# Kernel tuning notes

Hardware: AMD Instinct MI355X
Metric: run time of the kernel (lower is better)

The kernel has to match this reference:

```python
import jax, jax.numpy as jnp
import numpy as np

T = 32          # chain length (init arg)
K = 2048        # particles per timestep (Ks)
RES = 0.5       # observed scalar (init buffer)
LIKE_STD = 1.0  # likelihood std (init arg)
LOG2PI = float(np.log(2.0 * np.pi))


def _logpdf(x, mu, std):
    # Normal(mu, std).log_prob(x)
    z = (x - mu) / std
    return -0.5 * z * z - jnp.log(std) - 0.5 * LOG2PI


def logmmmeanexp(X, Y):
    # log( exp(X) @ exp(Y) / X.shape[1] ), numerically stabilized exactly as the torch code
    x = jnp.max(X, axis=1, keepdims=True)
    y = jnp.max(Y, axis=0, keepdims=True)
    return x + y + jnp.log(jnp.exp(X - x) @ jnp.exp(Y - y)) - jnp.log(jnp.asarray(X.shape[1], X.dtype))


def setup_inputs() -> dict:
    key = jax.random.key(0)
    eps = jax.random.normal(key, (T, K), dtype=jnp.float32)
    means = jnp.zeros((T,), jnp.float32)
    # matches the torch init: sqrt((1+arange(T))/T)
    log_stds = jnp.sqrt((1.0 + jnp.arange(T, dtype=jnp.float32)) / T)
    return {"means": means, "log_stds": log_stds, "eps": eps}


def reference(means, log_stds, eps):
    std = jnp.exp(log_stds)                            # proposal stds, (T,)
    zs = means[:, None] + std[:, None] * eps           # reparameterized samples, (T,K)
    log_q = _logpdf(zs, means[:, None], std[:, None])  # proposal log-probs, (T,K)
    sp = jnp.sqrt(1.0 / T)                             # prior/transition std

    # first factor: prior over z_0 minus proposal, (1,K)
    r0 = (_logpdf(zs[0], 0.0, sp) - log_q[0])[None, :]
    # middle factors: transition log-probs, (T-1, K, K); Ms[i][j,k] = logN(zs[i+1,k]; zs[i,j], sp) - log_q[i+1,k]
    Ms = _logpdf(zs[1:, None, :], zs[:-1, :, None], sp) - log_q[1:, None, :]

    def step(r, M):
        return logmmmeanexp(r, M), None

    r, _ = jax.lax.scan(step, r0, Ms)
    # likelihood factor, (K,1)
    L = _logpdf(jnp.float32(RES), zs[-1][:, None], jnp.float32(LIKE_STD))
    return logmmmeanexp(r, L)  # (1,1) log marginal-likelihood estimate
```

## Files before the change

### kernel.cpp

```cpp
#include <hip/hip_runtime.h>
#include <math.h>

#define T 32
#define K 2048
#define NBLOCKS 256
#define NTHREADS 512
#define HB 128
#define CPB 16
#define QS 4
#define SSTRIDE 32
#define L2E_F 1.4426950408889634f
#define LN2_F 0.6931471805599453f
#define LOG2PI_F 1.8378770664093453f
#define SP_F     0.17677669529663687f
#define LOG_SP_F (-1.7328679513998633f)
#define CNORM_F  (-(LOG_SP_F) - 0.5f * LOG2PI_F)

#if __has_builtin(__builtin_amdgcn_exp2f)
#define EXP2F(x) __builtin_amdgcn_exp2f(x)
#else
#define EXP2F(x) exp2f(x)
#endif
#if __has_builtin(__builtin_amdgcn_logf)
#define LOG2F(x) __builtin_amdgcn_logf(x)
#else
#define LOG2F(x) log2f(x)
#endif

__device__ __forceinline__ float aload4(const float* p) {
    return __hip_atomic_load(p, __ATOMIC_RELAXED, __HIP_MEMORY_SCOPE_AGENT);
}
__device__ __forceinline__ void astore4(float* p, float v) {
    __hip_atomic_store(p, v, __ATOMIC_RELAXED, __HIP_MEMORY_SCOPE_AGENT);
}
__device__ __forceinline__ void astore8(float* p, float a, float b) {
    union { float2 f; unsigned long long u; } v;
    v.f = make_float2(a, b);
    __hip_atomic_store((unsigned long long*)p, v.u, __ATOMIC_RELAXED,
                       __HIP_MEMORY_SCOPE_AGENT);
}
__device__ __forceinline__ int sload(const int* p) {
    return __hip_atomic_load(p, __ATOMIC_RELAXED, __HIP_MEMORY_SCOPE_AGENT);
}
__device__ __forceinline__ void sstore(int* p, int v) {
    __hip_atomic_store(p, v, __ATOMIC_RELAXED, __HIP_MEMORY_SCOPE_AGENT);
}

__global__ __launch_bounds__(NTHREADS) void fused_kernel(
    const float* __restrict__ means, const float* __restrict__ log_stds,
    const float* __restrict__ eps, float* __restrict__ fbuf,
    float* __restrict__ bbuf, int* __restrict__ fsent, int* __restrict__ bsent,
    float* __restrict__ out)
{
    __shared__ float2 shzD[2][K];
    __shared__ float2 lzc[T][CPB];
    __shared__ float smu[T], sstd[T], slq2[T];
    __shared__ float red[16];
    __shared__ int ldsflag;

    const int tid  = threadIdx.x;
    const int b    = blockIdx.x;
    const bool fwd = (b < HB);
    const int lb   = fwd ? b : b - HB;
    const int col0 = lb * CPB;

    if (tid == 0) ldsflag = 0;

    {
        int t = tid >> 4, dcol = tid & 15;
        float mu = means[t];
        float st = expf(log_stds[t]);
        if (dcol == 0) {
            smu[t] = mu; sstd[t] = st;
            slq2[t] = L2E_F * (logf(st) + 0.5f * LOG2PI_F);
        }
        float e = eps[t * K + col0 + dcol];
        float z = fmaf(st, e, mu);
        float log_q = fmaf(-0.5f * e, e, -logf(st) - 0.5f * LOG2PI_F);
        float tz2 = (32.0f * L2E_F) * z;
        if (fwd) {
            float cm2 = fmaf((-16.0f * L2E_F) * z, z,
                             L2E_F * (CNORM_F - log_q)) - 11.0f;
            lzc[t][dcol] = make_float2(tz2, cm2);
            if (t == 0) {
                float r0 = fmaf(-16.0f * z, z, CNORM_F) - log_q;
                astore4(&fbuf[col0 + dcol], r0 * L2E_F);
            }
        } else {
            float cm2 = fmaf((-16.0f * L2E_F) * z, z, L2E_F * CNORM_F) - 11.0f;
            lzc[t][dcol] = make_float2(tz2, cm2);
            if (t == T - 1) {
                float d = 0.5f - z;
                float c31 = fmaf(-0.5f * d, d, -0.5f * LOG2PI_F);
                astore4(&bbuf[col0 + dcol], c31 * L2E_F);
            }
        }
    }
    __syncthreads();
    int* mysent = fwd ? fsent : bsent;
    if (tid == 0) sstore(&mysent[lb * SSTRIDE], 1);

    const int lane = tid & 63;
    const int wave = tid >> 6;
    float* mybuf = fwd ? fbuf : bbuf;
    const int nstep = fwd ? 16 : 15;

    for (int p = 0; p < nstep; ++p) {
        const int par  = p & 1;
        const int need = p + 1;
        const int tin  = fwd ? p : 31 - p;
        const int town = fwd ? p + 1 : 30 - p;
        const float mu_i  = smu[tin];
        const float std_i = sstd[tin];
        const float lqc   = slq2[tin];
        const float* erow = eps + tin * K;

        float zloc[QS], dadd[QS];
        #pragma unroll
        for (int q = 0; q < QS; ++q) {
            float e = erow[tid + q * NTHREADS];
            float z = fmaf(std_i, e, mu_i);
            zloc[q] = z;
            float base = fwd ? 0.0f : fmaf((0.5f * L2E_F) * e, e, lqc);
            dadd[q] = fmaf((-16.0f * L2E_F) * z, z, base);
        }

        if (wave == 0) {
            const int* s0 = mysent + lane * SSTRIDE;
            const int* s1 = mysent + (lane + 64) * SSTRIDE;
            bool ok0 = false, ok1 = false;
            for (;;) {
                if (!ok0) ok0 = sload(s0) >= need;
                if (!ok1) ok1 = sload(s1) >= need;
                if (__all(ok0 & ok1)) break;
                __builtin_amdgcn_s_sleep(1);
            }
            __hip_atomic_store(&ldsflag, need, __ATOMIC_RELEASE,
                               __HIP_MEMORY_SCOPE_WORKGROUP);
        } else {
            while (__hip_atomic_load(&ldsflag, __ATOMIC_ACQUIRE,
                                     __HIP_MEMORY_SCOPE_WORKGROUP) < need)
                __builtin_amdgcn_s_sleep(1);
        }

        const float* mrow = mybuf + par * K;
        float rv[QS];
        #pragma unroll
        for (int q = 0; q < QS; ++q) rv[q] = aload4(&mrow[tid + q * NTHREADS]);
        #pragma unroll
        for (int q = 0; q < QS; ++q)
            shzD[par][tid + q * NTHREADS] = make_float2(zloc[q], rv[q] + dadd[q]);
        __syncthreads();

        const float4* shp = (const float4*)&shzD[par][0];
        float2 zcA = lzc[town][2 * wave];
        float2 zcB = lzc[town][2 * wave + 1];
        float4 fr[16];
        #pragma unroll
        for (int i = 0; i < 16; ++i) fr[i] = shp[lane + (i << 6)];
        float m0 = -INFINITY, m1 = -INFINITY;
        #pragma unroll
        for (int i = 0; i < 16; ++i) {
            m0 = fmaxf(m0, fmaxf(fmaf(zcA.x, fr[i].x, fr[i].y),
                                 fmaf(zcA.x, fr[i].z, fr[i].w)));
            m1 = fmaxf(m1, fmaxf(fmaf(zcB.x, fr[i].x, fr[i].y),
                                 fmaf(zcB.x, fr[i].z, fr[i].w)));
        }
        #pragma unroll
        for (int off = 32; off >= 1; off >>= 1) {
            m0 = fmaxf(m0, __shfl_xor(m0, off, 64));
            m1 = fmaxf(m1, __shfl_xor(m1, off, 64));
        }
        float s0 = 0.0f, s1 = 0.0f;
        #pragma unroll
        for (int i = 0; i < 16; ++i) {
            s0 += EXP2F(fmaf(zcA.x, fr[i].x, fr[i].y) - m0);
            s0 += EXP2F(fmaf(zcA.x, fr[i].z, fr[i].w) - m0);
            s1 += EXP2F(fmaf(zcB.x, fr[i].x, fr[i].y) - m1);
            s1 += EXP2F(fmaf(zcB.x, fr[i].z, fr[i].w) - m1);
        }
        #pragma unroll
        for (int off = 32; off >= 1; off >>= 1) {
            s0 += __shfl_xor(s0, off, 64);
            s1 += __shfl_xor(s1, off, 64);
        }
        if (lane == 0) {
            astore8(&mybuf[(par ^ 1) * K + col0 + 2 * wave],
                    zcA.y + m0 + LOG2F(s0), zcB.y + m1 + LOG2F(s1));
        }
        __syncthreads();
        if (tid == 0) sstore(&mysent[lb * SSTRIDE], p + 2);
    }

    if (b == 0) {
        {
            const int* f0 = fsent + lane * SSTRIDE;
            const int* f1 = fsent + (lane + 64) * SSTRIDE;
            const int* g0 = bsent + lane * SSTRIDE;
            const int* g1 = bsent + (lane + 64) * SSTRIDE;
            bool a0 = false, a1 = false, a2 = false, a3 = false;
            for (;;) {
                if (!a0) a0 = sload(f0) >= 17;
                if (!a1) a1 = sload(f1) >= 17;
                if (!a2) a2 = sload(g0) >= 16;
                if (!a3) a3 = sload(g1) >= 16;
                if (__all(a0 & a1 & a2 & a3)) break;
                __builtin_amdgcn_s_sleep(1);
            }
        }
        float vals[QS];
        float m = -INFINITY;
        #pragma unroll
        for (int q = 0; q < QS; ++q) {
            int j = tid + q * NTHREADS;
            float v = aload4(&fbuf[j]) + aload4(&bbuf[K + j]);
            vals[q] = v;
            m = fmaxf(m, v);
        }
        #pragma unroll
        for (int off = 32; off >= 1; off >>= 1) m = fmaxf(m, __shfl_xor(m, off, 64));
        float ssum = 0.0f;
        #pragma unroll
        for (int q = 0; q < QS; ++q) ssum += EXP2F(vals[q] - m);
        #pragma unroll
        for (int off = 32; off >= 1; off >>= 1) ssum += __shfl_xor(ssum, off, 64);
        if (lane == 0) { red[wave] = m; red[8 + wave] = ssum; }
        __syncthreads();
        if (tid == 0) {
            float m8 = -INFINITY;
            #pragma unroll
            for (int i = 0; i < 8; ++i) m8 = fmaxf(m8, red[i]);
            float s8 = 0.0f;
            #pragma unroll
            for (int i = 0; i < 8; ++i) s8 += red[8 + i] * EXP2F(red[i] - m8);
            out[0] = LN2_F * (m8 + LOG2F(s8) - 11.0f);
        }
    }
}

extern "C" void kernel_launch(void* const* d_in, const int* in_sizes, int n_in,
                              void* d_out, int out_size, void* d_ws, size_t ws_size,
                              hipStream_t stream) {
    const float* means    = (const float*)d_in[0];
    const float* log_stds = (const float*)d_in[1];
    const float* eps      = (const float*)d_in[2];
    float* out = (float*)d_out;

    float* fbuf = (float*)d_ws;
    float* bbuf = fbuf + 2 * K;
    int*   fsent = (int*)(bbuf + 2 * K);
    int*   bsent = fsent + 128 * SSTRIDE;

    fused_kernel<<<NBLOCKS, NTHREADS, 0, stream>>>(
        means, log_stds, eps, fbuf, bbuf, fsent, bsent, out);
}
```

Baseline: 115.0 us.

## Add aggregator block to centralize grid barrier and publish replicated ready flags

Adds a 257th block whose two waves poll the per-block forward and backward sentinels and publish one step counter per direction, replicated eight times at padded addresses. Worker blocks then spin on a single replicated flag instead of each polling all 128 sentinels of their half, which cuts L2 polling traffic. The trade-off is an extra hop of latency on every step, plus the aggregator's own polling. The 8-byte result store is also split into two 4-byte stores, and the final reduction waits on the aggregated flags.

```diff
diff --git a/kernel.cpp b/kernel.cpp
--- a/kernel.cpp
+++ b/kernel.cpp
@@ -3,12 +3,14 @@
 
 #define T 32
 #define K 2048
-#define NBLOCKS 256
+#define NWORK 256
+#define NBLK 257
 #define NTHREADS 512
 #define HB 128
 #define CPB 16
 #define QS 4
 #define SSTRIDE 32
+#define NFLREP 8
 #define L2E_F 1.4426950408889634f
 #define LN2_F 0.6931471805599453f
 #define LOG2PI_F 1.8378770664093453f
@@ -33,12 +35,6 @@
 __device__ __forceinline__ void astore4(float* p, float v) {
     __hip_atomic_store(p, v, __ATOMIC_RELAXED, __HIP_MEMORY_SCOPE_AGENT);
 }
-__device__ __forceinline__ void astore8(float* p, float a, float b) {
-    union { float2 f; unsigned long long u; } v;
-    v.f = make_float2(a, b);
-    __hip_atomic_store((unsigned long long*)p, v.u, __ATOMIC_RELAXED,
-                       __HIP_MEMORY_SCOPE_AGENT);
-}
 __device__ __forceinline__ int sload(const int* p) {
     return __hip_atomic_load(p, __ATOMIC_RELAXED, __HIP_MEMORY_SCOPE_AGENT);
 }
@@ -50,7 +46,7 @@
     const float* __restrict__ means, const float* __restrict__ log_stds,
     const float* __restrict__ eps, float* __restrict__ fbuf,
     float* __restrict__ bbuf, int* __restrict__ fsent, int* __restrict__ bsent,
-    float* __restrict__ out)
+    int* __restrict__ fflag, int* __restrict__ bflag, float* __restrict__ out)
 {
     __shared__ float2 shzD[2][K];
     __shared__ float2 lzc[T][CPB];
@@ -60,6 +56,38 @@
 
     const int tid  = threadIdx.x;
     const int b    = blockIdx.x;
+    const int lane = tid & 63;
+    const int wave = tid >> 6;
+
+    if (b == NWORK) {
+        if (wave == 0) {
+            const int* s0 = fsent + lane * SSTRIDE;
+            const int* s1 = fsent + (lane + 64) * SSTRIDE;
+            for (int need = 1; need <= 17; ++need) {
+                for (;;) {
+                    int v0 = sload(s0);
+                    int v1 = sload(s1);
+                    if (__all(min(v0, v1) >= need)) break;
+                    __builtin_amdgcn_s_sleep(1);
+                }
+                if (lane < NFLREP) sstore(&fflag[lane * SSTRIDE], need);
+            }
+        } else if (wave == 1) {
+            const int* s0 = bsent + lane * SSTRIDE;
+            const int* s1 = bsent + (lane + 64) * SSTRIDE;
+            for (int need = 1; need <= 16; ++need) {
+                for (;;) {
+                    int v0 = sload(s0);
+                    int v1 = sload(s1);
+                    if (__all(min(v0, v1) >= need)) break;
+                    __builtin_amdgcn_s_sleep(1);
+                }
+                if (lane < NFLREP) sstore(&bflag[lane * SSTRIDE], need);
+            }
+        }
+        return;
+    }
+
     const bool fwd = (b < HB);
     const int lb   = fwd ? b : b - HB;
     const int col0 = lb * CPB;
@@ -100,9 +128,8 @@
     int* mysent = fwd ? fsent : bsent;
     if (tid == 0) sstore(&mysent[lb * SSTRIDE], 1);
 
-    const int lane = tid & 63;
-    const int wave = tid >> 6;
     float* mybuf = fwd ? fbuf : bbuf;
+    const int* myflag = (fwd ? fflag : bflag) + (lb & (NFLREP - 1)) * SSTRIDE;
     const int nstep = fwd ? 16 : 15;
 
     for (int p = 0; p < nstep; ++p) {
@@ -126,13 +153,9 @@
         }
 
         if (wave == 0) {
-            const int* s0 = mysent + lane * SSTRIDE;
-            const int* s1 = mysent + (lane + 64) * SSTRIDE;
-            bool ok0 = false, ok1 = false;
             for (;;) {
-                if (!ok0) ok0 = sload(s0) >= need;
-                if (!ok1) ok1 = sload(s1) >= need;
-                if (__all(ok0 & ok1)) break;
+                int v = sload(myflag);
+                if (__all(v >= need)) break;
                 __builtin_amdgcn_s_sleep(1);
             }
             __hip_atomic_store(&ldsflag, need, __ATOMIC_RELEASE,
@@ -184,9 +207,12 @@
             s0 += __shfl_xor(s0, off, 64);
             s1 += __shfl_xor(s1, off, 64);
         }
-        if (lane == 0) {
-            astore8(&mybuf[(par ^ 1) * K + col0 + 2 * wave],
-                    zcA.y + m0 + LOG2F(s0), zcB.y + m1 + LOG2F(s1));
+        if (lane < 2) {
+            float mm = lane ? m1 : m0;
+            float sv = lane ? s1 : s0;
+            float cm = lane ? zcB.y : zcA.y;
+            astore4(&mybuf[(par ^ 1) * K + col0 + 2 * wave + lane],
+                    cm + mm + LOG2F(sv));
         }
         __syncthreads();
         if (tid == 0) sstore(&mysent[lb * SSTRIDE], p + 2);
@@ -194,17 +220,12 @@
 
     if (b == 0) {
         {
-            const int* f0 = fsent + lane * SSTRIDE;
-            const int* f1 = fsent + (lane + 64) * SSTRIDE;
-            const int* g0 = bsent + lane * SSTRIDE;
-            const int* g1 = bsent + (lane + 64) * SSTRIDE;
-            bool a0 = false, a1 = false, a2 = false, a3 = false;
+            const int* ff = fflag;
+            const int* bf = bflag;
             for (;;) {
-                if (!a0) a0 = sload(f0) >= 17;
-                if (!a1) a1 = sload(f1) >= 17;
-                if (!a2) a2 = sload(g0) >= 16;
-                if (!a3) a3 = sload(g1) >= 16;
-                if (__all(a0 & a1 & a2 & a3)) break;
+                int f = sload(ff);
+                int g = sload(bf);
+                if (__all((f >= 17) & (g >= 16))) break;
                 __builtin_amdgcn_s_sleep(1);
             }
         }
@@ -250,7 +271,9 @@
     float* bbuf = fbuf + 2 * K;
     int*   fsent = (int*)(bbuf + 2 * K);
     int*   bsent = fsent + 128 * SSTRIDE;
-
-    fused_kernel<<<NBLOCKS, NTHREADS, 0, stream>>>(
-        means, log_stds, eps, fbuf, bbuf, fsent, bsent, out);
-}
+    int*   fflag = bsent + 128 * SSTRIDE;
+    int*   bflag = fflag + NFLREP * SSTRIDE;
+
+    fused_kernel<<<NBLK, NTHREADS, 0, stream>>>(
+        means, log_stds, eps, fbuf, bbuf, fsent, bsent, fflag, bflag, out);
+}
```

Result: slower. 118.3 us (+2.9%).

## Replace sentinel flags with tagged value messages polled directly by each thread

Applied to the files above, without the earlier changes.

Each inter-block value is now sent as a 64-bit word holding the float result plus a step tag, and each step gets its own buffer slot. Consumers spin on the data itself rather than on per-block sentinels. This removes the wave-0 poll with the LDS flag hand-off, the trailing __syncthreads, and the separate sentinel store, cutting per-step synchronisation latency. In exchange it doubles message traffic, uses more workspace, and makes every thread poll global memory. Tags left in the workspace by a previous launch could satisfy a wait early.

```diff
diff --git a/kernel.cpp b/kernel.cpp
--- a/kernel.cpp
+++ b/kernel.cpp
@@ -8,11 +8,9 @@
 #define HB 128
 #define CPB 16
 #define QS 4
-#define SSTRIDE 32
 #define L2E_F 1.4426950408889634f
 #define LN2_F 0.6931471805599453f
 #define LOG2PI_F 1.8378770664093453f
-#define SP_F     0.17677669529663687f
 #define LOG_SP_F (-1.7328679513998633f)
 #define CNORM_F  (-(LOG_SP_F) - 0.5f * LOG2PI_F)
 
@@ -27,44 +25,38 @@
 #define LOG2F(x) log2f(x)
 #endif
 
-__device__ __forceinline__ float aload4(const float* p) {
+__device__ __forceinline__ unsigned long long aload8u(const unsigned long long* p) {
     return __hip_atomic_load(p, __ATOMIC_RELAXED, __HIP_MEMORY_SCOPE_AGENT);
 }
-__device__ __forceinline__ void astore4(float* p, float v) {
+__device__ __forceinline__ void astore8u(unsigned long long* p, unsigned long long v) {
     __hip_atomic_store(p, v, __ATOMIC_RELAXED, __HIP_MEMORY_SCOPE_AGENT);
 }
-__device__ __forceinline__ void astore8(float* p, float a, float b) {
-    union { float2 f; unsigned long long u; } v;
-    v.f = make_float2(a, b);
-    __hip_atomic_store((unsigned long long*)p, v.u, __ATOMIC_RELAXED,
-                       __HIP_MEMORY_SCOPE_AGENT);
-}
-__device__ __forceinline__ int sload(const int* p) {
-    return __hip_atomic_load(p, __ATOMIC_RELAXED, __HIP_MEMORY_SCOPE_AGENT);
-}
-__device__ __forceinline__ void sstore(int* p, int v) {
-    __hip_atomic_store(p, v, __ATOMIC_RELAXED, __HIP_MEMORY_SCOPE_AGENT);
+__device__ __forceinline__ unsigned long long packvt(float v, int tag) {
+    return ((unsigned long long)(unsigned)tag << 32) |
+           (unsigned long long)__float_as_uint(v);
+}
+__device__ __forceinline__ int tagof(unsigned long long u) { return (int)(u >> 32); }
+__device__ __forceinline__ float valof(unsigned long long u) {
+    return __uint_as_float((unsigned)u);
 }
 
 __global__ __launch_bounds__(NTHREADS) void fused_kernel(
     const float* __restrict__ means, const float* __restrict__ log_stds,
-    const float* __restrict__ eps, float* __restrict__ fbuf,
-    float* __restrict__ bbuf, int* __restrict__ fsent, int* __restrict__ bsent,
-    float* __restrict__ out)
+    const float* __restrict__ eps, unsigned long long* __restrict__ fmsg,
+    unsigned long long* __restrict__ bmsg, float* __restrict__ out)
 {
     __shared__ float2 shzD[2][K];
     __shared__ float2 lzc[T][CPB];
     __shared__ float smu[T], sstd[T], slq2[T];
     __shared__ float red[16];
-    __shared__ int ldsflag;
 
     const int tid  = threadIdx.x;
     const int b    = blockIdx.x;
+    const int lane = tid & 63;
+    const int wave = tid >> 6;
     const bool fwd = (b < HB);
     const int lb   = fwd ? b : b - HB;
     const int col0 = lb * CPB;
-
-    if (tid == 0) ldsflag = 0;
 
     {
         int t = tid >> 4, dcol = tid & 15;
@@ -84,7 +76,7 @@
             lzc[t][dcol] = make_float2(tz2, cm2);
             if (t == 0) {
                 float r0 = fmaf(-16.0f * z, z, CNORM_F) - log_q;
-                astore4(&fbuf[col0 + dcol], r0 * L2E_F);
+                astore8u(&fmsg[col0 + dcol], packvt(r0 * L2E_F, 1));
             }
         } else {
             float cm2 = fmaf((-16.0f * L2E_F) * z, z, L2E_F * CNORM_F) - 11.0f;
@@ -92,17 +84,13 @@
             if (t == T - 1) {
                 float d = 0.5f - z;
                 float c31 = fmaf(-0.5f * d, d, -0.5f * LOG2PI_F);
-                astore4(&bbuf[col0 + dcol], c31 * L2E_F);
+                astore8u(&bmsg[col0 + dcol], packvt(c31 * L2E_F, 1));
             }
         }
     }
     __syncthreads();
-    int* mysent = fwd ? fsent : bsent;
-    if (tid == 0) sstore(&mysent[lb * SSTRIDE], 1);
-
-    const int lane = tid & 63;
-    const int wave = tid >> 6;
-    float* mybuf = fwd ? fbuf : bbuf;
+
+    unsigned long long* mymsg = fwd ? fmsg : bmsg;
     const int nstep = fwd ? 16 : 15;
 
     for (int p = 0; p < nstep; ++p) {
@@ -125,31 +113,23 @@
             dadd[q] = fmaf((-16.0f * L2E_F) * z, z, base);
         }
 
-        if (wave == 0) {
-            const int* s0 = mysent + lane * SSTRIDE;
-            const int* s1 = mysent + (lane + 64) * SSTRIDE;
-            bool ok0 = false, ok1 = false;
-            for (;;) {
-                if (!ok0) ok0 = sload(s0) >= need;
-                if (!ok1) ok1 = sload(s1) >= need;
-                if (__all(ok0 & ok1)) break;
-                __builtin_amdgcn_s_sleep(1);
-            }
-            __hip_atomic_store(&ldsflag, need, __ATOMIC_RELEASE,
-                               __HIP_MEMORY_SCOPE_WORKGROUP);
-        } else {
-            while (__hip_atomic_load(&ldsflag, __ATOMIC_ACQUIRE,
-                                     __HIP_MEMORY_SCOPE_WORKGROUP) < need)
-                __builtin_amdgcn_s_sleep(1);
-        }
-
-        const float* mrow = mybuf + par * K;
-        float rv[QS];
-        #pragma unroll
-        for (int q = 0; q < QS; ++q) rv[q] = aload4(&mrow[tid + q * NTHREADS]);
-        #pragma unroll
-        for (int q = 0; q < QS; ++q)
-            shzD[par][tid + q * NTHREADS] = make_float2(zloc[q], rv[q] + dadd[q]);
+        const unsigned long long* mrow = mymsg + (size_t)p * K;
+        unsigned long long u0, u1, u2, u3;
+        for (;;) {
+            u0 = aload8u(mrow + tid);
+            u1 = aload8u(mrow + tid + NTHREADS);
+            u2 = aload8u(mrow + tid + 2 * NTHREADS);
+            u3 = aload8u(mrow + tid + 3 * NTHREADS);
+            bool v = (tagof(u0) == need) & (tagof(u1) == need) &
+                     (tagof(u2) == need) & (tagof(u3) == need);
+            if (__all(v)) break;
+            __builtin_amdgcn_s_sleep(1);
+        }
+
+        shzD[par][tid]                = make_float2(zloc[0], valof(u0) + dadd[0]);
+        shzD[par][tid + NTHREADS]     = make_float2(zloc[1], valof(u1) + dadd[1]);
+        shzD[par][tid + 2 * NTHREADS] = make_float2(zloc[2], valof(u2) + dadd[2]);
+        shzD[par][tid + 3 * NTHREADS] = make_float2(zloc[3], valof(u3) + dadd[3]);
         __syncthreads();
 
         const float4* shp = (const float4*)&shzD[par][0];
@@ -184,39 +164,41 @@
             s0 += __shfl_xor(s0, off, 64);
             s1 += __shfl_xor(s1, off, 64);
         }
-        if (lane == 0) {
-            astore8(&mybuf[(par ^ 1) * K + col0 + 2 * wave],
-                    zcA.y + m0 + LOG2F(s0), zcB.y + m1 + LOG2F(s1));
-        }
-        __syncthreads();
-        if (tid == 0) sstore(&mysent[lb * SSTRIDE], p + 2);
+        if (lane < 2) {
+            float mm = lane ? m1 : m0;
+            float sv = lane ? s1 : s0;
+            float cm = lane ? zcB.y : zcA.y;
+            astore8u(&mymsg[(size_t)(p + 1) * K + col0 + 2 * wave + lane],
+                     packvt(cm + mm + LOG2F(sv), p + 2));
+        }
     }
 
     if (b == 0) {
-        {
-            const int* f0 = fsent + lane * SSTRIDE;
-            const int* f1 = fsent + (lane + 64) * SSTRIDE;
-            const int* g0 = bsent + lane * SSTRIDE;
-            const int* g1 = bsent + (lane + 64) * SSTRIDE;
-            bool a0 = false, a1 = false, a2 = false, a3 = false;
-            for (;;) {
-                if (!a0) a0 = sload(f0) >= 17;
-                if (!a1) a1 = sload(f1) >= 17;
-                if (!a2) a2 = sload(g0) >= 16;
-                if (!a3) a3 = sload(g1) >= 16;
-                if (__all(a0 & a1 & a2 & a3)) break;
-                __builtin_amdgcn_s_sleep(1);
-            }
+        const unsigned long long* fr16 = fmsg + (size_t)16 * K;
+        const unsigned long long* br15 = bmsg + (size_t)15 * K;
+        unsigned long long a0, a1, a2, a3, c0, c1, c2, c3;
+        for (;;) {
+            a0 = aload8u(fr16 + tid);
+            a1 = aload8u(fr16 + tid + NTHREADS);
+            a2 = aload8u(fr16 + tid + 2 * NTHREADS);
+            a3 = aload8u(fr16 + tid + 3 * NTHREADS);
+            c0 = aload8u(br15 + tid);
+            c1 = aload8u(br15 + tid + NTHREADS);
+            c2 = aload8u(br15 + tid + 2 * NTHREADS);
+            c3 = aload8u(br15 + tid + 3 * NTHREADS);
+            bool v = (tagof(a0) == 17) & (tagof(a1) == 17) &
+                     (tagof(a2) == 17) & (tagof(a3) == 17) &
+                     (tagof(c0) == 16) & (tagof(c1) == 16) &
+                     (tagof(c2) == 16) & (tagof(c3) == 16);
+            if (__all(v)) break;
+            __builtin_amdgcn_s_sleep(1);
         }
         float vals[QS];
-        float m = -INFINITY;
-        #pragma unroll
-        for (int q = 0; q < QS; ++q) {
-            int j = tid + q * NTHREADS;
-            float v = aload4(&fbuf[j]) + aload4(&bbuf[K + j]);
-            vals[q] = v;
-            m = fmaxf(m, v);
-        }
+        vals[0] = valof(a0) + valof(c0);
+        vals[1] = valof(a1) + valof(c1);
+        vals[2] = valof(a2) + valof(c2);
+        vals[3] = valof(a3) + valof(c3);
+        float m = fmaxf(fmaxf(vals[0], vals[1]), fmaxf(vals[2], vals[3]));
         #pragma unroll
         for (int off = 32; off >= 1; off >>= 1) m = fmaxf(m, __shfl_xor(m, off, 64));
         float ssum = 0.0f;
@@ -246,11 +228,9 @@
     const float* eps      = (const float*)d_in[2];
     float* out = (float*)d_out;
 
-    float* fbuf = (float*)d_ws;
-    float* bbuf = fbuf + 2 * K;
-    int*   fsent = (int*)(bbuf + 2 * K);
-    int*   bsent = fsent + 128 * SSTRIDE;
+    unsigned long long* fmsg = (unsigned long long*)d_ws;
+    unsigned long long* bmsg = fmsg + (size_t)17 * K;
 
     fused_kernel<<<NBLOCKS, NTHREADS, 0, stream>>>(
-        means, log_stds, eps, fbuf, bbuf, fsent, bsent, out);
-}
+        means, log_stds, eps, fmsg, bmsg, out);
+}
```

Result: slower. 122.3 us (+6.4%).
